# Kernel optimization log

Hardware: AMD Instinct MI355X
Metric: run time of the kernel (lower is better)

The kernel has to match this reference:

```python
import jax, jax.numpy as jnp
import numpy as np

NUM_HEADS = 16
NUM_KV_HEADS = 4
HEAD_DIM = 128
EPS = 1e-6


def _rotate_half(x):
    x1, x2 = jnp.split(x, 2, axis=-1)
    return jnp.concatenate((-x2, x1), axis=-1)


def _rms_norm(x, w):
    var = jnp.mean(x * x, axis=-1, keepdims=True)
    return x * jax.lax.rsqrt(var + EPS) * w


def setup_inputs() -> dict:
    key = jax.random.key(0)
    ks = jax.random.split(key, 6)
    B, S, H = 2, 2048, 2048
    hidden_states = jax.random.normal(ks[0], (B, S, H), dtype=jnp.float32)
    # real RoPE tables (HF-style: freqs tiled twice along last dim)
    inv_freq = 1.0 / (10000.0 ** (np.arange(0, HEAD_DIM, 2, dtype=np.float32) / HEAD_DIM))
    pos = np.arange(S, dtype=np.float32)
    ang = np.concatenate([pos[:, None] * inv_freq[None, :]] * 2, axis=-1)  # [S, head_dim]
    cos = jnp.broadcast_to(jnp.cos(ang)[None], (B, S, HEAD_DIM)).astype(jnp.float32)
    sin = jnp.broadcast_to(jnp.sin(ang)[None], (B, S, HEAD_DIM)).astype(jnp.float32)
    sc = 0.02
    Wq = jax.random.normal(ks[1], (NUM_HEADS * HEAD_DIM, H), dtype=jnp.float32) * sc
    Wk = jax.random.normal(ks[2], (NUM_KV_HEADS * HEAD_DIM, H), dtype=jnp.float32) * sc
    Wv = jax.random.normal(ks[3], (NUM_KV_HEADS * HEAD_DIM, H), dtype=jnp.float32) * sc
    Wo = jax.random.normal(ks[4], (H, NUM_HEADS * HEAD_DIM), dtype=jnp.float32) * sc
    q_norm_w = jnp.ones((HEAD_DIM,), dtype=jnp.float32)
    k_norm_w = jnp.ones((HEAD_DIM,), dtype=jnp.float32)
    return {"hidden_states": hidden_states, "cos": cos, "sin": sin,
            "Wq": Wq, "Wk": Wk, "Wv": Wv, "Wo": Wo,
            "q_norm_w": q_norm_w, "k_norm_w": k_norm_w}


def reference(hidden_states, cos, sin, Wq, Wk, Wv, Wo, q_norm_w, k_norm_w):
    B, S, H = hidden_states.shape
    groups = NUM_HEADS // NUM_KV_HEADS
    # projections (Linear: x @ W^T), then [B, h, S, d]
    q = (hidden_states @ Wq.T).reshape(B, S, NUM_HEADS, HEAD_DIM).transpose(0, 2, 1, 3)
    k = (hidden_states @ Wk.T).reshape(B, S, NUM_KV_HEADS, HEAD_DIM).transpose(0, 2, 1, 3)
    v = (hidden_states @ Wv.T).reshape(B, S, NUM_KV_HEADS, HEAD_DIM).transpose(0, 2, 1, 3)
    # per-head RMSNorm
    q = _rms_norm(q, q_norm_w)
    k = _rms_norm(k, k_norm_w)
    # RoPE, cos/sin broadcast over heads (unsqueeze_dim=1)
    c = cos[:, None, :, :]
    s = sin[:, None, :, :]
    q = q * c + _rotate_half(q) * s
    k = k * c + _rotate_half(k) * s
    # GQA: expand kv heads
    k = jnp.repeat(k, groups, axis=1)
    v = jnp.repeat(v, groups, axis=1)
    scale = 1.0 / jnp.sqrt(jnp.float32(HEAD_DIM))
    scores = jnp.einsum('bhqd,bhkd->bhqk', q, k) * scale
    attn = jax.nn.softmax(scores, axis=-1)
    out = jnp.einsum('bhqk,bhkd->bhqd', attn, v)
    out = out.transpose(0, 2, 1, 3).reshape(B, S, NUM_HEADS * HEAD_DIM)
    return out @ Wo.T
```

## Files before the change

kernel.cpp:

```cpp
#include <hip/hip_runtime.h>
#include <hip/hip_bf16.h>
#include <stdint.h>

typedef __attribute__((ext_vector_type(8))) short short8;
typedef __attribute__((ext_vector_type(4))) float floatx4;

#define MFMA16(a, b, c) __builtin_amdgcn_mfma_f32_16x16x32_bf16(a, b, c, 0, 0, 0)

static __device__ __forceinline__ void gload_lds16(const __hip_bfloat16* g, __hip_bfloat16* l) {
  __builtin_amdgcn_global_load_lds(
      (const __attribute__((address_space(1))) void*)g,
      (__attribute__((address_space(3))) void*)l,
      16, 0, 0);
}

__global__ void f2bf(const float* __restrict__ in, __hip_bfloat16* __restrict__ out, int n) {
  const int stride = gridDim.x * blockDim.x * 4;
  for (int i = (blockIdx.x * blockDim.x + threadIdx.x) * 4; i < n; i += stride) {
    const float4 v = *(const float4*)(in + i);
    __hip_bfloat16 t[4] = {__float2bfloat16(v.x), __float2bfloat16(v.y),
                           __float2bfloat16(v.z), __float2bfloat16(v.w)};
    *(short4*)(out + i) = *(const short4*)t;
  }
}

template <typename OUT_T>
__global__ __launch_bounds__(256)
void gemm_bt(const __hip_bfloat16* __restrict__ A, const __hip_bfloat16* __restrict__ Bt,
             OUT_T* __restrict__ C, int M, int N, int K) {
  __shared__ __hip_bfloat16 As[2][128 * 32];
  __shared__ __hip_bfloat16 Bs[2][128 * 32];
  const int tid = threadIdx.x;
  const int wid = tid >> 6, lane = tid & 63;
  const int lg = lane >> 4, lr = lane & 15;
  const int wr = wid >> 1, wc = wid & 1;
  const int m0 = blockIdx.x * 128, n0 = blockIdx.y * 128;
  const int nk = K >> 5;

  floatx4 acc[4][4];
#pragma unroll
  for (int mi = 0; mi < 4; ++mi)
#pragma unroll
    for (int ni = 0; ni < 4; ++ni) acc[mi][ni] = (floatx4)(0.0f);

  auto stage = [&](int buf, int kt) {
    const int k0 = kt << 5;
#pragma unroll
    for (int i = 0; i < 2; ++i) {
      const int e = (i * 256 + tid) * 8;
      const int row = e >> 5, col = e & 31;
      gload_lds16(A + (size_t)(m0 + row) * K + k0 + col, &As[buf][e]);
    }
#pragma unroll
    for (int i = 0; i < 2; ++i) {
      const int e = (i * 256 + tid) * 8;
      const int row = e >> 5, col = e & 31;
      gload_lds16(Bt + (size_t)(n0 + row) * K + k0 + col, &Bs[buf][e]);
    }
  };

  stage(0, 0);
  __syncthreads();

  for (int kt = 0; kt < nk; ++kt) {
    const int cur = kt & 1;
    if (kt + 1 < nk) stage(cur ^ 1, kt + 1);
    short8 af[4], bfr[4];
#pragma unroll
    for (int mi = 0; mi < 4; ++mi)
      af[mi] = *(const short8*)&As[cur][(wr * 64 + mi * 16 + lr) * 32 + lg * 8];
#pragma unroll
    for (int ni = 0; ni < 4; ++ni)
      bfr[ni] = *(const short8*)&Bs[cur][(wc * 64 + ni * 16 + lr) * 32 + lg * 8];
#pragma unroll
    for (int mi = 0; mi < 4; ++mi)
#pragma unroll
      for (int ni = 0; ni < 4; ++ni) acc[mi][ni] = MFMA16(af[mi], bfr[ni], acc[mi][ni]);
    __syncthreads();
  }

#pragma unroll
  for (int mi = 0; mi < 4; ++mi)
#pragma unroll
    for (int ni = 0; ni < 4; ++ni) {
      const int row = m0 + wr * 64 + mi * 16 + lg * 4;
      const int col = n0 + wc * 64 + ni * 16 + lr;
#pragma unroll
      for (int r = 0; r < 4; ++r) {
        C[(size_t)(row + r) * N + col] = (OUT_T)acc[mi][ni][r];
      }
    }
}

__global__ __launch_bounds__(256)
void normrope(const __hip_bfloat16* __restrict__ qkv, const float* __restrict__ cosb,
              const float* __restrict__ sinb, const float* __restrict__ qw,
              const float* __restrict__ kw, __hip_bfloat16* __restrict__ Q,
              __hip_bfloat16* __restrict__ K, __hip_bfloat16* __restrict__ V) {
  const int m = blockIdx.x;
  const int b = m >> 11, s = m & 2047;
  const int wid = threadIdx.x >> 6, lane = threadIdx.x & 63;
  const size_t qkvrow = (size_t)m * 3072;
  const float c1 = cosb[(size_t)m * 128 + lane], s1 = sinb[(size_t)m * 128 + lane];
  const float c2 = cosb[(size_t)m * 128 + lane + 64], s2 = sinb[(size_t)m * 128 + lane + 64];
  for (int h = wid * 6; h < wid * 6 + 6; ++h) {
    const float x1 = __bfloat162float(qkv[qkvrow + h * 128 + lane]);
    const float x2 = __bfloat162float(qkv[qkvrow + h * 128 + lane + 64]);
    if (h < 20) {
      float ss = x1 * x1 + x2 * x2;
      ss += __shfl_xor(ss, 1);  ss += __shfl_xor(ss, 2);  ss += __shfl_xor(ss, 4);
      ss += __shfl_xor(ss, 8);  ss += __shfl_xor(ss, 16); ss += __shfl_xor(ss, 32);
      const float rs = rsqrtf(ss * (1.0f / 128.0f) + 1e-6f);
      const float* w = (h < 16) ? qw : kw;
      const float n1 = x1 * rs * w[lane], n2 = x2 * rs * w[lane + 64];
      const float o1 = n1 * c1 - n2 * s1;
      const float o2 = n2 * c2 + n1 * s2;
      if (h < 16) {
        const size_t base = ((size_t)(b * 16 + h) * 2048 + s) * 128;
        Q[base + lane] = __float2bfloat16(o1);
        Q[base + lane + 64] = __float2bfloat16(o2);
      } else {
        const size_t base = ((size_t)(b * 4 + h - 16) * 2048 + s) * 128;
        K[base + lane] = __float2bfloat16(o1);
        K[base + lane + 64] = __float2bfloat16(o2);
      }
    } else {
      const size_t base = ((size_t)(b * 4 + h - 20) * 2048 + s) * 128;
      V[base + lane] = qkv[qkvrow + h * 128 + lane];
      V[base + lane + 64] = qkv[qkvrow + h * 128 + lane + 64];
    }
  }
}

__global__ __launch_bounds__(256)
void vtrans(const __hip_bfloat16* __restrict__ V, __hip_bfloat16* __restrict__ Vt) {
  __shared__ short L[64 * 65];
  const int tid = threadIdx.x;
  const int s0 = blockIdx.x * 64, d0 = blockIdx.y * 64, bz = blockIdx.z;
  const __hip_bfloat16* src = V + (size_t)bz * 2048 * 128;
#pragma unroll
  for (int i = 0; i < 2; ++i) {
    const int slot = i * 256 + tid;
    const int srow = slot >> 3, c8 = (slot & 7) * 8;
    short8 v = *(const short8*)(src + (size_t)(s0 + srow) * 128 + d0 + c8);
#pragma unroll
    for (int j = 0; j < 8; ++j) L[(c8 + j) * 65 + srow] = v[j];
  }
  __syncthreads();
  __hip_bfloat16* dst = Vt + (size_t)bz * 128 * 2048;
#pragma unroll
  for (int i = 0; i < 2; ++i) {
    const int slot = i * 256 + tid;
    const int drow = slot >> 3, sc8 = (slot & 7) * 8;
    short8 o;
#pragma unroll
    for (int j = 0; j < 8; ++j) o[j] = L[drow * 65 + sc8 + j];
    *(short8*)(dst + (size_t)(d0 + drow) * 2048 + s0 + sc8) = o;
  }
}

__global__ __launch_bounds__(256, 2)
void fattn(const __hip_bfloat16* __restrict__ Qg, const __hip_bfloat16* __restrict__ Kg,
           const __hip_bfloat16* __restrict__ Vtg, __hip_bfloat16* __restrict__ Og) {
  __shared__ short Ksf[64 * 136];
  __shared__ short Vtl[128 * 72];
  __shared__ __hip_bfloat16 Ps[4][32][72];

  const int tid = threadIdx.x, wid = tid >> 6, lane = tid & 63;
  const int lg = lane >> 4, lr = lane & 15;
  const int qt = blockIdx.x, bh = blockIdx.y;
  const int b = bh >> 4, h = bh & 15, hkv = h >> 2;
  const int q0w = qt * 128 + wid * 32;

  short8 qf[2][4];
#pragma unroll
  for (int g = 0; g < 2; ++g) {
    const __hip_bfloat16* Qrow =
        Qg + ((size_t)((b * 16 + h) * 2048 + q0w + g * 16 + lr)) * 128;
#pragma unroll
    for (int ks = 0; ks < 4; ++ks) qf[g][ks] = *(const short8*)(Qrow + ks * 32 + lg * 8);
  }

  const __hip_bfloat16* Kbase = Kg + (size_t)(b * 4 + hkv) * 2048 * 128;
  const __hip_bfloat16* Vtbase = Vtg + (size_t)(b * 4 + hkv) * 128 * 2048;

  int koff[4], kldsoff[4], voff[4], vldsoff[4];
#pragma unroll
  for (int i = 0; i < 4; ++i) {
    const int idx = i * 256 + tid;
    const int kkv = idx >> 4, kd = (idx & 15) * 8;
    koff[i] = kkv * 128 + kd;
    kldsoff[i] = kkv * 136 + kd;
    const int vd = idx >> 3, vc = (idx & 7) * 8;
    voff[i] = vd * 2048 + vc;
    vldsoff[i] = vd * 72 + vc;
  }

  floatx4 oacc[2][8];
#pragma unroll
  for (int g = 0; g < 2; ++g)
#pragma unroll
    for (int nd = 0; nd < 8; ++nd) oacc[g][nd] = (floatx4)(0.0f);
  floatx4 lacc[2];
  lacc[0] = (floatx4)(0.0f);
  lacc[1] = (floatx4)(0.0f);

  short8 ones;
#pragma unroll
  for (int j = 0; j < 8; ++j) ones[j] = (short)0x3F80;

  const float scale = 0.08838834764831845f;

  short8 kreg[4], vreg[4];
  auto loadKV = [&](int kt) {
    const __hip_bfloat16* kp = Kbase + (size_t)kt * 64 * 128;
    const __hip_bfloat16* vp = Vtbase + (size_t)kt * 64;
#pragma unroll
    for (int i = 0; i < 4; ++i) kreg[i] = *(const short8*)(kp + koff[i]);
#pragma unroll
    for (int i = 0; i < 4; ++i) vreg[i] = *(const short8*)(vp + voff[i]);
  };

  loadKV(0);

  for (int kt = 0; kt < 32; ++kt) {
    if (kt) {
      asm volatile("s_waitcnt lgkmcnt(0)" ::: "memory");
      __builtin_amdgcn_s_barrier();
      __builtin_amdgcn_sched_barrier(0);
    }
#pragma unroll
    for (int i = 0; i < 4; ++i) *(short8*)&Ksf[kldsoff[i]] = kreg[i];
#pragma unroll
    for (int i = 0; i < 4; ++i) *(short8*)&Vtl[vldsoff[i]] = vreg[i];
    if (kt + 1 < 32) loadKV(kt + 1);
    asm volatile("s_waitcnt lgkmcnt(0)" ::: "memory");
    __builtin_amdgcn_s_barrier();
    __builtin_amdgcn_sched_barrier(0);

    floatx4 sacc[2][4];
#pragma unroll
    for (int g = 0; g < 2; ++g)
#pragma unroll
      for (int ni = 0; ni < 4; ++ni) sacc[g][ni] = (floatx4)(0.0f);
    __builtin_amdgcn_s_setprio(1);
#pragma unroll
    for (int ks = 0; ks < 4; ++ks) {
#pragma unroll
      for (int ni = 0; ni < 4; ++ni) {
        const short8 kf = *(const short8*)&Ksf[(ni * 16 + lr) * 136 + ks * 32 + lg * 8];
        sacc[0][ni] = MFMA16(qf[0][ks], kf, sacc[0][ni]);
        sacc[1][ni] = MFMA16(qf[1][ks], kf, sacc[1][ni]);
      }
    }
    __builtin_amdgcn_s_setprio(0);

#pragma unroll
    for (int g = 0; g < 2; ++g)
#pragma unroll
      for (int ni = 0; ni < 4; ++ni)
#pragma unroll
        for (int r = 0; r < 4; ++r) {
          const float p = __expf(sacc[g][ni][r] * scale - 12.0f);
          Ps[wid][g * 16 + lg * 4 + r][ni * 16 + lr] = __float2bfloat16(p);
        }

#pragma unroll
    for (int ks2 = 0; ks2 < 2; ++ks2) {
      const short8 pf0 = *(const short8*)&Ps[wid][lr][ks2 * 32 + lg * 8];
      const short8 pf1 = *(const short8*)&Ps[wid][16 + lr][ks2 * 32 + lg * 8];
      __builtin_amdgcn_s_setprio(1);
      lacc[0] = MFMA16(pf0, ones, lacc[0]);
      lacc[1] = MFMA16(pf1, ones, lacc[1]);
#pragma unroll
      for (int nd = 0; nd < 8; ++nd) {
        const short8 vf = *(const short8*)&Vtl[(nd * 16 + lr) * 72 + ks2 * 32 + lg * 8];
        oacc[0][nd] = MFMA16(pf0, vf, oacc[0][nd]);
        oacc[1][nd] = MFMA16(pf1, vf, oacc[1][nd]);
      }
      __builtin_amdgcn_s_setprio(0);
    }
  }

#pragma unroll
  for (int g = 0; g < 2; ++g)
#pragma unroll
    for (int r = 0; r < 4; ++r) {
      const float inv = 1.0f / lacc[g][r];
      const int s = q0w + g * 16 + lg * 4 + r;
      __hip_bfloat16* orow = Og + ((size_t)(b * 2048 + s)) * 2048 + h * 128;
#pragma unroll
      for (int nd = 0; nd < 8; ++nd)
        orow[nd * 16 + lr] = __float2bfloat16(oacc[g][nd][r] * inv);
    }
}

extern "C" void kernel_launch(void* const* d_in, const int* in_sizes, int n_in,
                              void* d_out, int out_size, void* d_ws, size_t ws_size,
                              hipStream_t stream) {
  const float* hidden = (const float*)d_in[0];
  const float* cosb = (const float*)d_in[1];
  const float* sinb = (const float*)d_in[2];
  const float* Wq = (const float*)d_in[3];
  const float* Wk = (const float*)d_in[4];
  const float* Wv = (const float*)d_in[5];
  const float* Wo = (const float*)d_in[6];
  const float* qw = (const float*)d_in[7];
  const float* kw = (const float*)d_in[8];

  char* ws = (char*)d_ws;
  __hip_bfloat16* hidden_bf = (__hip_bfloat16*)ws; ws += (size_t)4096 * 2048 * 2;
  __hip_bfloat16* wqkv = (__hip_bfloat16*)ws;      ws += (size_t)3072 * 2048 * 2;
  __hip_bfloat16* wo_bf = (__hip_bfloat16*)ws;     ws += (size_t)2048 * 2048 * 2;
  __hip_bfloat16* qkv = (__hip_bfloat16*)ws;       ws += (size_t)4096 * 3072 * 2;
  __hip_bfloat16* Qb = (__hip_bfloat16*)ws;        ws += (size_t)2 * 16 * 2048 * 128 * 2;
  __hip_bfloat16* Kb = (__hip_bfloat16*)ws;        ws += (size_t)2 * 4 * 2048 * 128 * 2;
  __hip_bfloat16* Vb = (__hip_bfloat16*)ws;        ws += (size_t)2 * 4 * 2048 * 128 * 2;
  __hip_bfloat16* attn = (__hip_bfloat16*)ws;      ws += (size_t)4096 * 2048 * 2;
  __hip_bfloat16* Vt = wqkv;

  f2bf<<<1024, 256, 0, stream>>>(hidden, hidden_bf, 4096 * 2048);
  f2bf<<<1024, 256, 0, stream>>>(Wq, wqkv, 2048 * 2048);
  f2bf<<<512, 256, 0, stream>>>(Wk, wqkv + (size_t)2048 * 2048, 512 * 2048);
  f2bf<<<512, 256, 0, stream>>>(Wv, wqkv + (size_t)2560 * 2048, 512 * 2048);
  f2bf<<<1024, 256, 0, stream>>>(Wo, wo_bf, 2048 * 2048);

  gemm_bt<__hip_bfloat16><<<dim3(32, 24), 256, 0, stream>>>(hidden_bf, wqkv, qkv, 4096, 3072, 2048);
  normrope<<<4096, 256, 0, stream>>>(qkv, cosb, sinb, qw, kw, Qb, Kb, Vb);
  vtrans<<<dim3(32, 2, 8), 256, 0, stream>>>(Vb, Vt);
  fattn<<<dim3(16, 32), 256, 0, stream>>>(Qb, Kb, Vt, attn);
  gemm_bt<float><<<dim3(32, 16), 256, 0, stream>>>(attn, wo_bf, (float*)d_out, 4096, 2048, 2048);
}
```

Measured before the change: 240.0 us.

## Rewrite attention core with 32x32 MFMA and register-resident probabilities

Moves the flash-attention inner loops from 16x16x32 to 32x32x16 bf16 MFMA. S is computed transposed (K as the A operand) so P can be packed to bf16 with v_cvt_pk_bf16_f32 and rearranged across lane halves with shuffles, which removes the per-wave LDS round-trip for P. The epilogue stages output in LDS so global stores are coalesced 16-byte writes. It uses exp2 with a folded scale and a fixed offset and keeps normalisation without a running max, as before, and adds shuffle and select work in exchange for fewer LDS accesses.

```diff
diff --git a/kernel.cpp b/kernel.cpp
--- a/kernel.cpp
+++ b/kernel.cpp
@@ -4,8 +4,10 @@
 
 typedef __attribute__((ext_vector_type(8))) short short8;
 typedef __attribute__((ext_vector_type(4))) float floatx4;
+typedef __attribute__((ext_vector_type(16))) float floatx16;
 
 #define MFMA16(a, b, c) __builtin_amdgcn_mfma_f32_16x16x32_bf16(a, b, c, 0, 0, 0)
+#define MFMA32(a, b, c) __builtin_amdgcn_mfma_f32_32x32x16_bf16(a, b, c, 0, 0, 0)
 
 static __device__ __forceinline__ void gload_lds16(const __hip_bfloat16* g, __hip_bfloat16* l) {
   __builtin_amdgcn_global_load_lds(
@@ -162,24 +164,20 @@
 __global__ __launch_bounds__(256, 2)
 void fattn(const __hip_bfloat16* __restrict__ Qg, const __hip_bfloat16* __restrict__ Kg,
            const __hip_bfloat16* __restrict__ Vtg, __hip_bfloat16* __restrict__ Og) {
-  __shared__ short Ksf[64 * 136];
-  __shared__ short Vtl[128 * 72];
-  __shared__ __hip_bfloat16 Ps[4][32][72];
+  __shared__ short SMEM[17920];
+  short* Ksf = SMEM;
+  short* Vtl = SMEM + 8704;
 
   const int tid = threadIdx.x, wid = tid >> 6, lane = tid & 63;
-  const int lg = lane >> 4, lr = lane & 15;
+  const int l31 = lane & 31, hi = lane >> 5;
   const int qt = blockIdx.x, bh = blockIdx.y;
   const int b = bh >> 4, h = bh & 15, hkv = h >> 2;
   const int q0w = qt * 128 + wid * 32;
 
-  short8 qf[2][4];
-#pragma unroll
-  for (int g = 0; g < 2; ++g) {
-    const __hip_bfloat16* Qrow =
-        Qg + ((size_t)((b * 16 + h) * 2048 + q0w + g * 16 + lr)) * 128;
-#pragma unroll
-    for (int ks = 0; ks < 4; ++ks) qf[g][ks] = *(const short8*)(Qrow + ks * 32 + lg * 8);
-  }
+  const __hip_bfloat16* Qrow = Qg + ((size_t)((b * 16 + h) * 2048 + q0w + l31)) * 128;
+  short8 qf2[8];
+#pragma unroll
+  for (int ks = 0; ks < 8; ++ks) qf2[ks] = *(const short8*)(Qrow + ks * 16 + hi * 8);
 
   const __hip_bfloat16* Kbase = Kg + (size_t)(b * 4 + hkv) * 2048 * 128;
   const __hip_bfloat16* Vtbase = Vtg + (size_t)(b * 4 + hkv) * 128 * 2048;
@@ -196,20 +194,17 @@
     vldsoff[i] = vd * 72 + vc;
   }
 
-  floatx4 oacc[2][8];
-#pragma unroll
-  for (int g = 0; g < 2; ++g)
-#pragma unroll
-    for (int nd = 0; nd < 8; ++nd) oacc[g][nd] = (floatx4)(0.0f);
-  floatx4 lacc[2];
-  lacc[0] = (floatx4)(0.0f);
-  lacc[1] = (floatx4)(0.0f);
+  floatx16 oacc[4];
+#pragma unroll
+  for (int dblk = 0; dblk < 4; ++dblk) oacc[dblk] = (floatx16)(0.0f);
+  floatx16 lacc = (floatx16)(0.0f);
 
   short8 ones;
 #pragma unroll
   for (int j = 0; j < 8; ++j) ones[j] = (short)0x3F80;
 
-  const float scale = 0.08838834764831845f;
+  const float SC2 = 0.12753102497113446f;
+  const float OFF2 = 17.31234049066756f;
 
   short8 kreg[4], vreg[4];
   auto loadKV = [&](int kt) {
@@ -238,61 +233,79 @@
     __builtin_amdgcn_s_barrier();
     __builtin_amdgcn_sched_barrier(0);
 
-    floatx4 sacc[2][4];
-#pragma unroll
-    for (int g = 0; g < 2; ++g)
-#pragma unroll
-      for (int ni = 0; ni < 4; ++ni) sacc[g][ni] = (floatx4)(0.0f);
+    floatx16 st[2];
+    st[0] = (floatx16)(0.0f);
+    st[1] = (floatx16)(0.0f);
     __builtin_amdgcn_s_setprio(1);
 #pragma unroll
-    for (int ks = 0; ks < 4; ++ks) {
-#pragma unroll
-      for (int ni = 0; ni < 4; ++ni) {
-        const short8 kf = *(const short8*)&Ksf[(ni * 16 + lr) * 136 + ks * 32 + lg * 8];
-        sacc[0][ni] = MFMA16(qf[0][ks], kf, sacc[0][ni]);
-        sacc[1][ni] = MFMA16(qf[1][ks], kf, sacc[1][ni]);
+    for (int ks = 0; ks < 8; ++ks) {
+      const short8 kf0 = *(const short8*)&Ksf[l31 * 136 + ks * 16 + hi * 8];
+      const short8 kf1 = *(const short8*)&Ksf[(32 + l31) * 136 + ks * 16 + hi * 8];
+      st[0] = MFMA32(kf0, qf2[ks], st[0]);
+      st[1] = MFMA32(kf1, qf2[ks], st[1]);
+    }
+    __builtin_amdgcn_s_setprio(0);
+
+    int pk[2][4][2];
+#pragma unroll
+    for (int kvblk = 0; kvblk < 2; ++kvblk)
+#pragma unroll
+      for (int a = 0; a < 4; ++a)
+#pragma unroll
+        for (int i = 0; i < 2; ++i) {
+          const float e0 = exp2f(fmaf(st[kvblk][4 * a + 2 * i], SC2, -OFF2));
+          const float e1 = exp2f(fmaf(st[kvblk][4 * a + 2 * i + 1], SC2, -OFF2));
+          asm("v_cvt_pk_bf16_f32 %0, %1, %2" : "=v"(pk[kvblk][a][i]) : "v"(e0), "v"(e1));
+        }
+
+#pragma unroll
+    for (int kvblk = 0; kvblk < 2; ++kvblk) {
+#pragma unroll
+      for (int ks2 = 0; ks2 < 2; ++ks2) {
+        const int x0 = pk[kvblk][2 * ks2][0], x1 = pk[kvblk][2 * ks2][1];
+        const int y0 = pk[kvblk][2 * ks2 + 1][0], y1 = pk[kvblk][2 * ks2 + 1][1];
+        const int sx0 = __shfl_xor(x0, 32), sx1 = __shfl_xor(x1, 32);
+        const int sy0 = __shfl_xor(y0, 32), sy1 = __shfl_xor(y1, 32);
+        union { int i[4]; short8 s; } u;
+        u.i[0] = hi ? sy0 : x0;
+        u.i[1] = hi ? sy1 : x1;
+        u.i[2] = hi ? y0 : sx0;
+        u.i[3] = hi ? y1 : sx1;
+        const short8 pB = u.s;
+        __builtin_amdgcn_s_setprio(1);
+        lacc = MFMA32(ones, pB, lacc);
+#pragma unroll
+        for (int dblk = 0; dblk < 4; ++dblk) {
+          const short8 vf =
+              *(const short8*)&Vtl[(dblk * 32 + l31) * 72 + kvblk * 32 + ks2 * 16 + hi * 8];
+          oacc[dblk] = MFMA32(vf, pB, oacc[dblk]);
+        }
+        __builtin_amdgcn_s_setprio(0);
       }
     }
-    __builtin_amdgcn_s_setprio(0);
-
-#pragma unroll
-    for (int g = 0; g < 2; ++g)
-#pragma unroll
-      for (int ni = 0; ni < 4; ++ni)
-#pragma unroll
-        for (int r = 0; r < 4; ++r) {
-          const float p = __expf(sacc[g][ni][r] * scale - 12.0f);
-          Ps[wid][g * 16 + lg * 4 + r][ni * 16 + lr] = __float2bfloat16(p);
-        }
-
-#pragma unroll
-    for (int ks2 = 0; ks2 < 2; ++ks2) {
-      const short8 pf0 = *(const short8*)&Ps[wid][lr][ks2 * 32 + lg * 8];
-      const short8 pf1 = *(const short8*)&Ps[wid][16 + lr][ks2 * 32 + lg * 8];
-      __builtin_amdgcn_s_setprio(1);
-      lacc[0] = MFMA16(pf0, ones, lacc[0]);
-      lacc[1] = MFMA16(pf1, ones, lacc[1]);
-#pragma unroll
-      for (int nd = 0; nd < 8; ++nd) {
-        const short8 vf = *(const short8*)&Vtl[(nd * 16 + lr) * 72 + ks2 * 32 + lg * 8];
-        oacc[0][nd] = MFMA16(pf0, vf, oacc[0][nd]);
-        oacc[1][nd] = MFMA16(pf1, vf, oacc[1][nd]);
-      }
-      __builtin_amdgcn_s_setprio(0);
-    }
-  }
-
-#pragma unroll
-  for (int g = 0; g < 2; ++g)
-#pragma unroll
-    for (int r = 0; r < 4; ++r) {
-      const float inv = 1.0f / lacc[g][r];
-      const int s = q0w + g * 16 + lg * 4 + r;
-      __hip_bfloat16* orow = Og + ((size_t)(b * 2048 + s)) * 2048 + h * 128;
-#pragma unroll
-      for (int nd = 0; nd < 8; ++nd)
-        orow[nd * 16 + lr] = __float2bfloat16(oacc[g][nd][r] * inv);
-    }
+  }
+
+  asm volatile("s_waitcnt lgkmcnt(0)" ::: "memory");
+  __builtin_amdgcn_s_barrier();
+
+  const float inv = 1.0f / lacc[0];
+  short* tw = SMEM + wid * 4352;
+#pragma unroll
+  for (int dblk = 0; dblk < 4; ++dblk)
+#pragma unroll
+    for (int a = 0; a < 4; ++a) {
+      __hip_bfloat16 o4[4];
+#pragma unroll
+      for (int r = 0; r < 4; ++r) o4[r] = __float2bfloat16(oacc[dblk][4 * a + r] * inv);
+      *(short4*)&tw[l31 * 136 + dblk * 32 + a * 8 + hi * 4] = *(const short4*)o4;
+    }
+  __hip_bfloat16* orow =
+      Og + ((size_t)(b * 2048 + q0w + (lane >> 1))) * 2048 + h * 128 + (lane & 1) * 64;
+  const short* trow = &tw[(lane >> 1) * 136 + (lane & 1) * 64];
+#pragma unroll
+  for (int c = 0; c < 8; ++c) {
+    *(short8*)(orow + c * 8) = *(const short8*)(trow + c * 8);
+  }
 }
 
 extern "C" void kernel_launch(void* const* d_in, const int* in_sizes, int n_in,
```

Measured after the change: 250.7 us. 4.5% more time.
